# Kernel optimization log

Hardware: AMD Instinct MI355X
Metric: run time of the kernel (lower is better)

The kernel has to match this reference:

```python
import jax, jax.numpy as jnp
import numpy as np

B_, N, C, H = 512, 49, 256, 8
DH = C // H            # 32
RB, NRF = 8, 32
NWIN = B_ // RB        # 64
DC = 64                # class_token_dim
TC = C + 2 * DC        # 384
WS = 7
SCALE = DH ** -0.5


def _rel_pos_index():
    ch = np.arange(WS)
    coords = np.stack(np.meshgrid(ch, ch, indexing='ij')).reshape(2, -1)  # [2,49]
    rel = (coords[:, :, None] - coords[:, None, :]).transpose(1, 2, 0)    # [49,49,2]
    rel[..., 0] += WS - 1
    rel[..., 1] += WS - 1
    rel[..., 0] *= 2 * WS - 1
    return jnp.asarray(rel.sum(-1).reshape(-1))  # [49*49]


def _ln(x, axes, eps=1e-5):
    m = x.mean(axes, keepdims=True)
    v = x.var(axes, keepdims=True)
    return (x - m) * jax.lax.rsqrt(v + eps)


def setup_inputs() -> dict:
    key = jax.random.key(0)
    ks = jax.random.split(key, 20)
    def w(i, shape, s=0.02):
        return jax.random.normal(ks[i], shape, jnp.float32) * s
    return dict(
        x=w(0, (B_, N, C), 1.0),
        x_ref=w(1, (RB, NRF, C), 1.0),
        depth_token=w(2, (B_, N, DC), 1.0),
        seg_token=w(3, (B_, N, DC), 1.0),
        qkv_w=w(4, (C, 3 * C)), qkv_b=jnp.zeros(3 * C, jnp.float32),
        proj_w=w(5, (C, C)), proj_b=jnp.zeros(C, jnp.float32),
        rel_bias=w(6, ((2 * WS - 1) ** 2, H)),
        diff_mu=w(7, (1, 1, C), 1.0), diff_logsigma=w(8, (1, 1, C)),
        ref_qk_w=w(9, (C, 2 * C)), ref_qk_b=jnp.zeros(2 * C, jnp.float32),
        conv_w=w(10, (H, H, 3, 3), 0.1), conv_b=jnp.zeros(H, jnp.float32),
        q_norm_w=jnp.ones(C, jnp.float32), q_norm_b=jnp.zeros(C, jnp.float32),
        q_proj_w=w(11, (C, C)), q_proj_b=jnp.zeros(C, jnp.float32),
        cls_dth_q_w=w(12, (DC, DC)), cls_dth_q_b=jnp.zeros(DC, jnp.float32),
        cls_seg_q_w=w(13, (DC, DC)), cls_seg_q_b=jnp.zeros(DC, jnp.float32),
        global_k_w=w(14, (TC, TC)), global_k_b=jnp.zeros(TC, jnp.float32),
        global_v_w=w(15, (TC, TC)), global_v_b=jnp.zeros(TC, jnp.float32),
        proj_dth_w=w(16, (DC, DC)), proj_dth_b=jnp.zeros(DC, jnp.float32),
    )


def reference(x, x_ref, depth_token, seg_token, qkv_w, qkv_b, proj_w, proj_b,
              rel_bias, diff_mu, diff_logsigma, ref_qk_w, ref_qk_b, conv_w, conv_b,
              q_norm_w, q_norm_b, q_proj_w, q_proj_b, cls_dth_q_w, cls_dth_q_b,
              cls_seg_q_w, cls_seg_q_b, global_k_w, global_k_b, global_v_w,
              global_v_b, proj_dth_w, proj_dth_b):
    # qkv: [B_,N,3C] -> q,k,v each [B_,H,N,DH]
    qkv = (x @ qkv_w + qkv_b).reshape(B_, N, 3, H, DH).transpose(2, 0, 3, 1, 4)
    q, k, v = qkv[0], qkv[1], qkv[2]

    # ---- group attention (ref branch) ----
    ref_qk = (x_ref @ ref_qk_w + ref_qk_b).reshape(RB, NRF, 2, C).transpose(2, 0, 1, 3)
    ref_q, ref_v = ref_qk[0], ref_qk[1]                       # [RB,NRF,C]
    ref_q = diff_mu + jnp.exp(diff_logsigma) * ref_q
    ref_q = ref_q.reshape(RB, NRF, H, DH).transpose(0, 2, 1, 3)  # [RB,H,NRF,DH]
    ref_v = ref_v.reshape(RB, NRF, H, DH).transpose(0, 2, 1, 3)

    qs = (q * SCALE).reshape(RB, NWIN, H, N, DH)
    # scores against shared (per-image) ref keys; avoids materializing repeated K
    ref_attn = jnp.einsum('rwhnd,rhfd->rhwnf', qs, ref_q)     # [RB,H,NWIN,N,NRF]
    ref_attn_r = ref_attn.reshape(RB, H, NWIN * N, NRF)
    # 3-step diffusion: conv2d over heads-as-channels + LN(no affine) + gelu, residual
    for _ in range(3):
        u = jax.lax.conv_general_dilated(
            ref_attn_r, conv_w, (1, 1), 'SAME',
            dimension_numbers=('NCHW', 'OIHW', 'NCHW')) + conv_b[None, :, None, None]
        u = jax.nn.gelu(_ln(u, (-2, -1)), approximate=False)
        ref_attn_r = ref_attn_r + u
    ref_attn = jax.nn.softmax(ref_attn_r.reshape(RB, H, NWIN, N, NRF), axis=-1)
    q_new = jnp.einsum('rhwnf,rhfd->rwnhd', ref_attn, ref_v).reshape(B_, N, C)
    q_sc = q.transpose(0, 2, 1, 3).reshape(B_, N, C)          # unscaled shortcut
    q_new = (_ln(q_new + q_sc, (-1,)) * q_norm_w + q_norm_b) @ q_proj_w + q_proj_b + q_sc
    q_new = q_new.reshape(B_, N, H, DH).transpose(0, 2, 1, 3) * SCALE

    # ---- window attention with relative position bias ----
    bias = rel_bias[_rel_pos_index()].reshape(N, N, H).transpose(2, 0, 1)  # [H,N,N]
    attn = jax.nn.softmax(jnp.einsum('bhnd,bhmd->bhnm', q_new, k) + bias[None], axis=-1)
    out = jnp.einsum('bhnm,bhmd->bnhd', attn, v).reshape(B_, N, C)
    out = out @ proj_w + proj_b

    # ---- class-token global attention ----
    dch = DC // H   # 8
    tdh = TC // H   # 48
    depth_q = (depth_token @ cls_dth_q_w + cls_dth_q_b).reshape(B_, N, H, dch).transpose(0, 2, 1, 3) * SCALE
    seg_q = (seg_token @ cls_seg_q_w + cls_seg_q_b).reshape(B_, N, H, dch).transpose(0, 2, 1, 3) * SCALE
    t_x = jnp.concatenate([out, depth_token, seg_token], axis=-1)  # [B_,N,TC]
    t_k = (t_x @ global_k_w + global_k_b).reshape(B_, N, H, tdh).transpose(0, 2, 1, 3)
    t_v = (t_x @ global_v_w + global_v_b).reshape(B_, N, H, tdh).transpose(0, 2, 1, 3)

    d_attn = jax.nn.softmax(jnp.einsum('bhnc,bhnt->bhct', depth_q, t_k), axis=-1)
    d_tok = jnp.einsum('bhct,bhnt->bhcn', d_attn, t_v).reshape(B_, DC, N).transpose(0, 2, 1)
    d_tok = d_tok @ proj_dth_w + proj_dth_b
    s_attn = jax.nn.softmax(jnp.einsum('bhnc,bhnt->bhct', seg_q, t_k), axis=-1)
    s_tok = jnp.einsum('bhct,bhnt->bhcn', s_attn, t_v).reshape(B_, DC, N).transpose(0, 2, 1)
    s_tok = s_tok @ proj_dth_w + proj_dth_b  # NOTE: original uses proj_dth for seg too
    return out, d_tok, s_tok
```

## Files before the change

### kernel.cpp

```cpp
#include <hip/hip_runtime.h>
#include <hip/hip_bf16.h>

typedef __hip_bfloat16 bf16;
typedef short s16x8 __attribute__((ext_vector_type(8)));
typedef float f32x4 __attribute__((ext_vector_type(4)));
union V16 { uint4 u4; s16x8 s8; unsigned u[4]; unsigned short s[8]; };

static __device__ __forceinline__ float b2f(bf16 v){ return __bfloat162float(v); }
static __device__ __forceinline__ bf16  f2b(float v){ return __float2bfloat16(v); }
static __device__ __forceinline__ unsigned short f2bs(float x){
    union { float f; unsigned u; } c; c.f = x;
    unsigned r = c.u + 0x7fff + ((c.u >> 16) & 1);
    return (unsigned short)(r >> 16);
}
static __device__ __forceinline__ float bu2f(unsigned short b){
    union { unsigned u; float f; } c; c.u = ((unsigned)b) << 16; return c.f;
}
static __device__ __forceinline__ s16x8 ld16g(const bf16* p){
    V16 u; u.u4 = *(const uint4*)p; return u.s8;
}
static __device__ __forceinline__ void glds16(const void* g, void* l){
    __builtin_amdgcn_global_load_lds(
        (const __attribute__((address_space(1))) unsigned*)g,
        (__attribute__((address_space(3))) unsigned*)l, 16, 0, 0);
}

#define SCALE_T 0.17677669529663687f

__global__ __launch_bounds__(256) void prep_weights(
    const float* __restrict__ qkvw, const float* __restrict__ qpw,
    const float* __restrict__ pw,   const float* __restrict__ gkw,
    const float* __restrict__ gvw,  bf16* __restrict__ Wt)
{
    int idx = blockIdx.x * 256 + threadIdx.x;
    float v;
    if (idx < 196608)      { int j = idx;          int n = j >> 8, k = j & 255; v = qkvw[k * 768 + n]; }
    else if (idx < 262144) { int j = idx - 196608; int n = j >> 8, k = j & 255; v = qpw[k * 256 + n]; }
    else if (idx < 327680) { int j = idx - 262144; int n = j >> 8, k = j & 255; v = pw[k * 256 + n]; }
    else if (idx < 475136) { int j = idx - 327680; int n = j / 384, k = j - n * 384; v = gkw[k * 384 + n]; }
    else                   { int j = idx - 475136; int n = j / 384, k = j - n * 384; v = gvw[k * 384 + n]; }
    ((unsigned short*)Wt)[idx] = f2bs(v);
}

__global__ __launch_bounds__(256) void convert_f32_bf16(
    const float* __restrict__ in, bf16* __restrict__ out)
{
    int i = blockIdx.x * 256 + threadIdx.x;
    float4 v = ((const float4*)in)[i];
    ushort4 o;
    o.x = f2bs(v.x); o.y = f2bs(v.y); o.z = f2bs(v.z); o.w = f2bs(v.w);
    ((ushort4*)out)[i] = o;
}

template<int TOK>
__global__ __launch_bounds__(256, 4) void gemm_bb(
    const bf16* __restrict__ A, int lda,
    const float* __restrict__ tokD, const float* __restrict__ tokS,
    const bf16* __restrict__ Wt, const float* __restrict__ bias,
    const float* __restrict__ bias2,
    const bf16* __restrict__ addp, int addStride,
    float* __restrict__ outF, bf16* __restrict__ outB, int outStrideB,
    int K, int N, float scale)
{
    __shared__ char lds[2][16384];

    const int tid = threadIdx.x;
    const int wv = tid >> 6, lane = tid & 63;
    const int quad = lane >> 4, l15 = lane & 15;
    const int wr = wv >> 1, wc = wv & 1;

    const int gx = (int)gridDim.x;
    const int nwg = gx * (int)gridDim.y;
    int bid = (int)blockIdx.y * gx + (int)blockIdx.x;
    if ((nwg & 7) == 0) bid = (bid & 7) * (nwg >> 3) + (bid >> 3);
    const int bx = bid % gx, by = bid / gx;
    const int rowBase = by * 128, colBase = bx * 128;

    const int srow = tid >> 2;
    const int kOffE = (((tid & 3) ^ ((srow >> 1) & 3)) << 3);

    const unsigned swz = (unsigned)((quad ^ ((l15 >> 1) & 3)) << 4);
    const unsigned aoff0 = (unsigned)(wr * 4096 + l15 * 64) + swz;
    const unsigned boff0 = (unsigned)(wc * 4096 + l15 * 64) + swz;

    f32x4 acc[4][4];
    #pragma unroll
    for (int m = 0; m < 4; ++m)
        #pragma unroll
        for (int n = 0; n < 4; ++n)
            #pragma unroll
            for (int r = 0; r < 4; ++r) acc[m][n][r] = 0.f;

    auto stage = [&](int sbuf, int kt) {
        char* base = &lds[sbuf][0];
        #pragma unroll
        for (int c = 0; c < 2; ++c)
            glds16(Wt + (size_t)(colBase + c * 64 + srow) * K + (kt + kOffE),
                   base + 8192 + c * 4096 + tid * 16);
        if (!TOK || kt < 256) {
            #pragma unroll
            for (int c = 0; c < 2; ++c)
                glds16(A + (size_t)(rowBase + c * 64 + srow) * lda + (kt + kOffE),
                       base + c * 4096 + tid * 16);
        } else {
            #pragma unroll
            for (int c = 0; c < 2; ++c) {
                int row = rowBase + c * 64 + srow;
                const float* sf = (kt < 320)
                    ? (tokD + (size_t)row * 64 + (kt - 256 + kOffE))
                    : (tokS + (size_t)row * 64 + (kt - 320 + kOffE));
                float4 u0 = ((const float4*)sf)[0];
                float4 u1 = ((const float4*)sf)[1];
                V16 o;
                o.s[0] = f2bs(u0.x); o.s[1] = f2bs(u0.y);
                o.s[2] = f2bs(u0.z); o.s[3] = f2bs(u0.w);
                o.s[4] = f2bs(u1.x); o.s[5] = f2bs(u1.y);
                o.s[6] = f2bs(u1.z); o.s[7] = f2bs(u1.w);
                *(uint4*)(base + c * 4096 + tid * 16) = o.u4;
            }
        }
    };

    stage(0, 0);
    __syncthreads();
    int buf = 0;
    for (int kt = 0; kt < K; kt += 32) {
        if (kt + 32 < K) stage(buf ^ 1, kt + 32);
        const char* Ab2 = &lds[buf][0];
        const char* Bb2 = Ab2 + 8192;
        s16x8 af[4], bfr[4];
        #pragma unroll
        for (int m = 0; m < 4; ++m) af[m]  = *(const s16x8*)(Ab2 + aoff0 + m * 1024);
        #pragma unroll
        for (int n = 0; n < 4; ++n) bfr[n] = *(const s16x8*)(Bb2 + boff0 + n * 1024);
        #pragma unroll
        for (int m = 0; m < 4; ++m)
            #pragma unroll
            for (int n = 0; n < 4; ++n)
                acc[m][n] = __builtin_amdgcn_mfma_f32_16x16x32_bf16(af[m], bfr[n], acc[m][n], 0, 0, 0);
        __syncthreads();
        buf ^= 1;
    }

    if (outB) {
        #pragma unroll
        for (int n = 0; n < 4; ++n) {
            int col = colBase + wc * 64 + n * 16 + l15;
            float bb = bias2 ? (col < 384 ? bias[col] : bias2[col - 384]) : bias[col];
            #pragma unroll
            for (int m = 0; m < 4; ++m) {
                #pragma unroll
                for (int r = 0; r < 4; ++r) {
                    int rl = wr * 64 + m * 16 + quad * 4 + r;
                    float v = acc[m][n][r] + bb;
                    if (addp) v += b2f(addp[(size_t)(rowBase + rl) * addStride + col]);
                    v *= scale;
                    if (outF) outF[(size_t)(rowBase + rl) * N + col] = v;
                    int cbyte = (wc * 64 + n * 16 + l15) * 2;
                    int blk = ((cbyte >> 5) ^ ((rl >> 2) & 7)) & 7;
                    *(unsigned short*)((char*)lds + rl * 256 + (blk << 5) + (cbyte & 31)) = f2bs(v);
                }
            }
        }
        __syncthreads();
        #pragma unroll
        for (int i = 0; i < 8; ++i) {
            int lin = i * 256 + tid;
            int rl = lin >> 4, cb = lin & 15;
            int cb2 = ((((cb >> 1) ^ ((rl >> 2) & 7)) & 7) << 1) | (cb & 1);
            uint4 val = *(const uint4*)((const char*)lds + rl * 256 + cb2 * 16);
            *(uint4*)(outB + (size_t)(rowBase + rl) * outStrideB + colBase + cb * 8) = val;
        }
    } else {
        #pragma unroll
        for (int n = 0; n < 4; ++n) {
            int col = colBase + wc * 64 + n * 16 + l15;
            float bb = bias2 ? (col < 384 ? bias[col] : bias2[col - 384]) : bias[col];
            #pragma unroll
            for (int m = 0; m < 4; ++m) {
                #pragma unroll
                for (int r = 0; r < 4; ++r) {
                    int rl = wr * 64 + m * 16 + quad * 4 + r;
                    float v = acc[m][n][r] + bb;
                    if (addp) v += b2f(addp[(size_t)(rowBase + rl) * addStride + col]);
                    v *= scale;
                    if (outF) outF[(size_t)(rowBase + rl) * N + col] = v;
                }
            }
        }
    }
}

__global__ __launch_bounds__(256) void mfma_gemm(
    const void* __restrict__ A, int a_mode,
    const float* __restrict__ Xd, const float* __restrict__ Xs,
    const float* __restrict__ W, const float* __restrict__ bias,
    const bf16* __restrict__ addp, int addStride,
    float* __restrict__ outF, bf16* __restrict__ outB,
    int M, int K, int N, float scale)
{
    __shared__ __hip_bfloat16 Al[64][48];
    __shared__ __hip_bfloat16 Bl[64][48];

    const int tid  = threadIdx.x;
    const int wv   = tid >> 6, lane = tid & 63;
    const int quad = lane >> 4, l15 = lane & 15;
    const int rowBase = blockIdx.y * 64, colBase = blockIdx.x * 64;

    const int am = tid >> 2, ak = (tid & 3) * 8;
    const int bn = tid & 63, bk = (tid >> 6) * 8;

    f32x4 acc[4];
    #pragma unroll
    for (int t = 0; t < 4; ++t)
        #pragma unroll
        for (int r = 0; r < 4; ++r) acc[t][r] = 0.f;

    for (int kt = 0; kt < K; kt += 32) {
        s16x8 sa;
        if (a_mode == 1) {
            const bf16* Ab = (const bf16*)A;
            V16 u; u.u4 = *(const uint4*)(Ab + (size_t)(rowBase + am) * K + kt + ak);
            sa = u.s8;
        } else {
            const float* src; size_t base;
            if (a_mode == 0) {
                src = (const float*)A; base = (size_t)(rowBase + am) * K + kt + ak;
            } else {
                int kcol = kt + ak;
                if (kcol < 256)      { src = (const float*)A; base = (size_t)(rowBase + am) * 256 + kcol; }
                else if (kcol < 320) { src = Xd; base = (size_t)(rowBase + am) * 64 + (kcol - 256); }
                else                 { src = Xs; base = (size_t)(rowBase + am) * 64 + (kcol - 320); }
            }
            const float4* p = (const float4*)(src + base);
            float4 u0 = p[0], u1 = p[1];
            sa[0] = (short)f2bs(u0.x); sa[1] = (short)f2bs(u0.y);
            sa[2] = (short)f2bs(u0.z); sa[3] = (short)f2bs(u0.w);
            sa[4] = (short)f2bs(u1.x); sa[5] = (short)f2bs(u1.y);
            sa[6] = (short)f2bs(u1.z); sa[7] = (short)f2bs(u1.w);
        }
        *(s16x8*)&Al[am][ak] = sa;

        s16x8 sb;
        #pragma unroll
        for (int j = 0; j < 8; ++j)
            sb[j] = (short)f2bs(W[(size_t)(kt + bk + j) * N + colBase + bn]);
        *(s16x8*)&Bl[bn][bk] = sb;

        __syncthreads();

        s16x8 a = *(const s16x8*)&Al[wv * 16 + l15][quad * 8];
        #pragma unroll
        for (int t = 0; t < 4; ++t) {
            s16x8 b = *(const s16x8*)&Bl[t * 16 + l15][quad * 8];
            acc[t] = __builtin_amdgcn_mfma_f32_16x16x32_bf16(a, b, acc[t], 0, 0, 0);
        }
        __syncthreads();
    }

    #pragma unroll
    for (int t = 0; t < 4; ++t) {
        int col = colBase + t * 16 + l15;
        float bb = bias[col];
        #pragma unroll
        for (int r = 0; r < 4; ++r) {
            int row = rowBase + wv * 16 + quad * 4 + r;
            float v = acc[t][r] + bb;
            if (addp) v += b2f(addp[(size_t)row * addStride + col]);
            v *= scale;
            if (outF) outF[(size_t)row * N + col] = v;
            if (outB) outB[(size_t)row * N + col] = f2b(v);
        }
    }
}

__global__ __launch_bounds__(256) void refprep_kernel(
    const float* __restrict__ ref_qk, const float* __restrict__ mu,
    const float* __restrict__ ls, float* __restrict__ ref_q_t,
    float* __restrict__ ref_v_t)
{
    int idx = blockIdx.x * 256 + threadIdx.x;
    int d = idx & 31, f = (idx >> 5) & 31, h = (idx >> 10) & 7, r = idx >> 13;
    int c = h * 32 + d;
    size_t src = (size_t)(r * 32 + f) * 512 + c;
    ref_q_t[idx] = mu[c] + __expf(ls[c]) * ref_qk[src];
    ref_v_t[idx] = ref_qk[src + 256];
}

__global__ __launch_bounds__(256) void refattn_kernel(
    const bf16* __restrict__ qkv, const float* __restrict__ ref_q_t,
    bf16* __restrict__ ref_attn)
{
    int blk = blockIdx.x;
    int w = blk & 63, h = (blk >> 6) & 7, r = blk >> 9;
    int b = r * 64 + w;
    __shared__ float qt[49 * 32];
    __shared__ float rq[32 * 33];
    int tid = threadIdx.x;
    for (int l = tid; l < 1568; l += 256) {
        int n = l >> 5, d = l & 31;
        qt[l] = b2f(qkv[(size_t)(b * 49 + n) * 768 + h * 32 + d]) * SCALE_T;
    }
    for (int l = tid; l < 1024; l += 256) {
        int f = l >> 5, d = l & 31;
        rq[f * 33 + d] = ref_q_t[(size_t)((r * 8 + h) * 32 + f) * 32 + d];
    }
    __syncthreads();
    for (int l = tid; l < 1568; l += 256) {
        int n = l >> 5, f = l & 31;
        float acc = 0.f;
        #pragma unroll
        for (int d2 = 0; d2 < 32; ++d2) acc += qt[n * 32 + d2] * rq[f * 33 + d2];
        ref_attn[(size_t)(((r * 8 + h) * 64 + w) * 49 + n) * 32 + f] = f2b(acc);
    }
}

__global__ __launch_bounds__(256) void conv_kernel(
    const bf16* __restrict__ in, const float* __restrict__ conv_w,
    const float* __restrict__ conv_b, bf16* __restrict__ u)
{
    __shared__ float w_s[576];
    __shared__ float b_s[8];
    int tid = threadIdx.x;
    for (int l = tid; l < 576; l += 256) w_s[l] = conv_w[l];
    if (tid < 8) b_s[tid] = conv_b[tid];
    __syncthreads();

    int idx = blockIdx.x * 256 + tid;
    int fb = idx & 3;
    int p  = (idx >> 2) % 3136;
    int r  = idx / 12544;
    int f0 = fb * 8;

    float acc[8][8];
    #pragma unroll
    for (int o = 0; o < 8; ++o) {
        float bo = b_s[o];
        #pragma unroll
        for (int f = 0; f < 8; ++f) acc[o][f] = bo;
    }

    for (int i = 0; i < 8; ++i) {
        float ext[3][10];
        #pragma unroll
        for (int dy = 0; dy < 3; ++dy) {
            int pp = p + dy - 1;
            bool pv = (unsigned)pp < 3136u;
            size_t base = ((size_t)((r * 8 + i) * 3136 + (pv ? pp : 0))) * 32 + f0;
            V16 uv;
            uv.u4 = pv ? *(const uint4*)(in + base) : make_uint4(0, 0, 0, 0);
            #pragma unroll
            for (int j = 0; j < 8; ++j) {
                unsigned sh = uv.u[j >> 1];
                unsigned bits = (j & 1) ? (sh & 0xffff0000u) : (sh << 16);
                union { unsigned uu; float fl; } cv; cv.uu = bits;
                ext[dy][j + 1] = cv.fl;
            }
            ext[dy][0] = (pv && f0 > 0)      ? b2f(in[base - 1]) : 0.f;
            ext[dy][9] = (pv && f0 + 8 < 32) ? b2f(in[base + 8]) : 0.f;
        }
        #pragma unroll
        for (int o = 0; o < 8; ++o) {
            #pragma unroll
            for (int ky = 0; ky < 3; ++ky) {
                const float* wp = &w_s[((o * 8 + i) * 3 + ky) * 3];
                float w0 = wp[0], w1 = wp[1], w2 = wp[2];
                #pragma unroll
                for (int f = 0; f < 8; ++f)
                    acc[o][f] += ext[ky][f] * w0 + ext[ky][f + 1] * w1 + ext[ky][f + 2] * w2;
            }
        }
    }

    #pragma unroll
    for (int o = 0; o < 8; ++o) {
        bf16 ov[8];
        #pragma unroll
        for (int f = 0; f < 8; ++f) ov[f] = f2b(acc[o][f]);
        *(uint4*)(u + ((size_t)((r * 8 + o) * 3136 + p)) * 32 + f0) = *(uint4*)ov;
    }
}

__global__ __launch_bounds__(256) void lnstats_kernel(
    const bf16* __restrict__ u, float* __restrict__ stats4)
{
    int g4 = blockIdx.x;
    const bf16* p = u + (size_t)g4 * 25088;
    int tid = threadIdx.x;
    float s = 0.f, s2 = 0.f;
    for (int it = tid; it < 3136; it += 256) {
        V16 uv; uv.u4 = *(const uint4*)(p + it * 8);
        #pragma unroll
        for (int j = 0; j < 8; ++j) {
            unsigned sh = uv.u[j >> 1];
            unsigned bits = (j & 1) ? (sh & 0xffff0000u) : (sh << 16);
            union { unsigned uu; float fl; } cv; cv.uu = bits;
            s += cv.fl; s2 += cv.fl * cv.fl;
        }
    }
    __shared__ float r1[256], r2[256];
    r1[tid] = s; r2[tid] = s2; __syncthreads();
    for (int st = 128; st > 0; st >>= 1) {
        if (tid < st) { r1[tid] += r1[tid + st]; r2[tid] += r2[tid + st]; }
        __syncthreads();
    }
    if (tid == 0) {
        stats4[g4 * 2]     = r1[0];
        stats4[g4 * 2 + 1] = r2[0];
    }
}

__global__ __launch_bounds__(256) void lngelu_kernel(
    const bf16* __restrict__ u, const float* __restrict__ stats4,
    bf16* __restrict__ ref_attn)
{
    int idx8 = blockIdx.x * 256 + threadIdx.x;
    int g = idx8 / 12544;
    size_t base = (size_t)idx8 * 8;
    float sum = 0.f, sq = 0.f;
    #pragma unroll
    for (int q = 0; q < 4; ++q) {
        sum += stats4[(g * 4 + q) * 2];
        sq  += stats4[(g * 4 + q) * 2 + 1];
    }
    float mean = sum * (1.f / 100352.f);
    float var  = sq * (1.f / 100352.f) - mean * mean;
    var = fmaxf(var, 0.f);
    float rstd = rsqrtf(var + 1e-5f);
    V16 uv; uv.u4 = *(const uint4*)(u + base);
    V16 rv; rv.u4 = *(const uint4*)(ref_attn + base);
    bf16 outv[8];
    #pragma unroll
    for (int j = 0; j < 8; ++j) {
        unsigned shu = uv.u[j >> 1];
        unsigned shr = rv.u[j >> 1];
        unsigned bu = (j & 1) ? (shu & 0xffff0000u) : (shu << 16);
        unsigned br = (j & 1) ? (shr & 0xffff0000u) : (shr << 16);
        union { unsigned uu; float fl; } cu, cr; cu.uu = bu; cr.uu = br;
        float v = (cu.fl - mean) * rstd;
        float ge = 0.5f * v * (1.f + erff(v * 0.7071067811865476f));
        outv[j] = f2b(cr.fl + ge);
    }
    *(uint4*)(ref_attn + base) = *(uint4*)outv;
}

__global__ __launch_bounds__(256) void qnew_pre_kernel(
    const bf16* __restrict__ qkv, const bf16* __restrict__ ref_attn,
    const float* __restrict__ ref_v_t,
    const float* __restrict__ qnw, const float* __restrict__ qnb,
    bf16* __restrict__ ln_t)
{
    int ww = threadIdx.x >> 6, lane = threadIdx.x & 63;
    int row = blockIdx.x * 4 + ww;
    int b = row / 49, n = row % 49;
    int r = b >> 6, w = b & 63;
    int h = lane >> 3, d0 = (lane & 7) * 4;

    const bf16* la = ref_attn + ((size_t)(((r * 8 + h) * 64 + w) * 49 + n)) * 32 + d0;
    ushort4 lu = *(const ushort4*)la;
    float lg[4] = { bu2f(lu.x), bu2f(lu.y), bu2f(lu.z), bu2f(lu.w) };

    float m = fmaxf(fmaxf(lg[0], lg[1]), fmaxf(lg[2], lg[3]));
    m = fmaxf(m, __shfl_xor(m, 1));
    m = fmaxf(m, __shfl_xor(m, 2));
    m = fmaxf(m, __shfl_xor(m, 4));
    float p[4], s = 0.f;
    #pragma unroll
    for (int j = 0; j < 4; ++j) { p[j] = __expf(lg[j] - m); s += p[j]; }
    s += __shfl_xor(s, 1);
    s += __shfl_xor(s, 2);
    s += __shfl_xor(s, 4);
    float inv = 1.f / s;
    #pragma unroll
    for (int j = 0; j < 4; ++j) p[j] *= inv;

    const float* rv = ref_v_t + ((size_t)(r * 8 + h) * 32) * 32 + d0;
    float y[4] = {0.f, 0.f, 0.f, 0.f};
    #pragma unroll
    for (int f = 0; f < 32; ++f) {
        int src = (lane & 56) | (f >> 2);
        float pf = __shfl(p[f & 3], src);
        float4 rvf = *(const float4*)(rv + f * 32);
        y[0] += pf * rvf.x; y[1] += pf * rvf.y;
        y[2] += pf * rvf.z; y[3] += pf * rvf.w;
    }

    ushort4 qu = *(const ushort4*)(qkv + (size_t)row * 768 + lane * 4);
    float z[4] = { y[0] + bu2f(qu.x), y[1] + bu2f(qu.y),
                   y[2] + bu2f(qu.z), y[3] + bu2f(qu.w) };

    float s1 = z[0] + z[1] + z[2] + z[3];
    #pragma unroll
    for (int off = 1; off < 64; off <<= 1) s1 += __shfl_xor(s1, off);
    float mean = s1 * (1.f / 256.f);
    float zc[4] = { z[0] - mean, z[1] - mean, z[2] - mean, z[3] - mean };
    float s2 = zc[0]*zc[0] + zc[1]*zc[1] + zc[2]*zc[2] + zc[3]*zc[3];
    #pragma unroll
    for (int off = 1; off < 64; off <<= 1) s2 += __shfl_xor(s2, off);
    float rstd = rsqrtf(s2 * (1.f / 256.f) + 1e-5f);

    float4 wv = *(const float4*)(qnw + lane * 4);
    float4 bv = *(const float4*)(qnb + lane * 4);
    bf16 outv[4];
    outv[0] = f2b(zc[0] * rstd * wv.x + bv.x);
    outv[1] = f2b(zc[1] * rstd * wv.y + bv.y);
    outv[2] = f2b(zc[2] * rstd * wv.z + bv.z);
    outv[3] = f2b(zc[3] * rstd * wv.w + bv.w);
    *(ushort4*)(ln_t + (size_t)row * 256 + lane * 4) = *(ushort4*)outv;
}

__global__ __launch_bounds__(256) void winattn_kernel(
    const bf16* __restrict__ qkv, const bf16* __restrict__ q_new,
    const float* __restrict__ rel_bias, bf16* __restrict__ attn_out)
{
    const int wv = threadIdx.x >> 6, lane = threadIdx.x & 63;
    const int quad = lane >> 4, l15 = lane & 15;
    const int b = blockIdx.x >> 1;
    const int h = (blockIdx.x & 1) * 4 + wv;

    __shared__ bf16 lds[4 * 6912];
    bf16* P  = &lds[wv * 6912];
    bf16* vT = P + 4608;

    {
        int m = lane;
        if (m < 49) {
            const bf16* vp = qkv + ((size_t)(b * 49 + m)) * 768 + 512 + h * 32;
            V16 v0, v1, v2, v3;
            v0.u4 = *(const uint4*)(vp);
            v1.u4 = *(const uint4*)(vp + 8);
            v2.u4 = *(const uint4*)(vp + 16);
            v3.u4 = *(const uint4*)(vp + 24);
            #pragma unroll
            for (int d = 0; d < 8; ++d) {
                ((unsigned short*)vT)[d * 72 + m]        = v0.s[d];
                ((unsigned short*)vT)[(d + 8) * 72 + m]  = v1.s[d];
                ((unsigned short*)vT)[(d + 16) * 72 + m] = v2.s[d];
                ((unsigned short*)vT)[(d + 24) * 72 + m] = v3.s[d];
            }
        } else {
            #pragma unroll
            for (int d = 0; d < 32; ++d)
                ((unsigned short*)vT)[d * 72 + m] = 0;
        }
    }

    s16x8 aq[4], bk[4];
    #pragma unroll
    for (int t = 0; t < 4; ++t) {
        int qr = t * 16 + l15; qr = qr > 48 ? 48 : qr;
        aq[t] = ld16g(q_new + ((size_t)(b * 49 + qr)) * 256 + h * 32 + quad * 8);
        bk[t] = ld16g(qkv + ((size_t)(b * 49 + qr)) * 768 + 256 + h * 32 + quad * 8);
    }
    f32x4 S[4][4];
    #pragma unroll
    for (int tn = 0; tn < 4; ++tn)
        #pragma unroll
        for (int tm = 0; tm < 4; ++tm) {
            #pragma unroll
            for (int r = 0; r < 4; ++r) S[tn][tm][r] = 0.f;
            S[tn][tm] = __builtin_amdgcn_mfma_f32_16x16x32_bf16(aq[tn], bk[tm], S[tn][tm], 0, 0, 0);
        }

    int mvalid[4], mi[4], mj[4];
    #pragma unroll
    for (int tm = 0; tm < 4; ++tm) {
        int m0 = tm * 16 + l15;
        mvalid[tm] = (m0 < 49);
        int mc = m0 > 48 ? 48 : m0;
        mi[tm] = mc / 7; mj[tm] = mc - mi[tm] * 7;
    }
    #pragma unroll
    for (int tn = 0; tn < 4; ++tn) {
        #pragma unroll
        for (int r = 0; r < 4; ++r) {
            int n0 = tn * 16 + quad * 4 + r;
            int nc = n0 > 48 ? 48 : n0;
            int ni = nc / 7, nj = nc - (nc / 7) * 7;
            float vals[4];
            float mx = -1e30f;
            #pragma unroll
            for (int tm = 0; tm < 4; ++tm) {
                float v = S[tn][tm][r]
                        + rel_bias[((ni - mi[tm] + 6) * 13 + (nj - mj[tm] + 6)) * 8 + h];
                if (!mvalid[tm]) v = -1e30f;
                vals[tm] = v;
                mx = fmaxf(mx, v);
            }
            mx = fmaxf(mx, __shfl_xor(mx, 1));
            mx = fmaxf(mx, __shfl_xor(mx, 2));
            mx = fmaxf(mx, __shfl_xor(mx, 4));
            mx = fmaxf(mx, __shfl_xor(mx, 8));
            float s = 0.f;
            #pragma unroll
            for (int tm = 0; tm < 4; ++tm) { vals[tm] = __expf(vals[tm] - mx); s += vals[tm]; }
            s += __shfl_xor(s, 1);
            s += __shfl_xor(s, 2);
            s += __shfl_xor(s, 4);
            s += __shfl_xor(s, 8);
            float inv = 1.f / s;
            #pragma unroll
            for (int tm = 0; tm < 4; ++tm)
                ((unsigned short*)P)[n0 * 72 + tm * 16 + l15] = f2bs(vals[tm] * inv);
        }
    }

    f32x4 O[4][2];
    #pragma unroll
    for (int tn = 0; tn < 4; ++tn)
        #pragma unroll
        for (int td = 0; td < 2; ++td)
            #pragma unroll
            for (int r = 0; r < 4; ++r) O[tn][td][r] = 0.f;

    #pragma unroll
    for (int ks = 0; ks < 2; ++ks) {
        s16x8 bv0 = *(const s16x8*)&vT[(0 * 16 + l15) * 72 + ks * 32 + quad * 8];
        s16x8 bv1 = *(const s16x8*)&vT[(1 * 16 + l15) * 72 + ks * 32 + quad * 8];
        #pragma unroll
        for (int tn = 0; tn < 4; ++tn) {
            s16x8 ap = *(const s16x8*)&P[(tn * 16 + l15) * 72 + ks * 32 + quad * 8];
            O[tn][0] = __builtin_amdgcn_mfma_f32_16x16x32_bf16(ap, bv0, O[tn][0], 0, 0, 0);
            O[tn][1] = __builtin_amdgcn_mfma_f32_16x16x32_bf16(ap, bv1, O[tn][1], 0, 0, 0);
        }
    }

    #pragma unroll
    for (int tn = 0; tn < 4; ++tn)
        #pragma unroll
        for (int r = 0; r < 4; ++r) {
            int n0 = tn * 16 + quad * 4 + r;
            if (n0 < 49) {
                size_t base = ((size_t)(b * 49 + n0)) * 256 + h * 32;
                attn_out[base + l15]      = f2b(O[tn][0][r]);
                attn_out[base + 16 + l15] = f2b(O[tn][1][r]);
            }
        }
}

__global__ __launch_bounds__(256) void clsattn_kernel(
    const bf16* __restrict__ tkv,
    const bf16* __restrict__ depth_q, const bf16* __restrict__ seg_q,
    bf16* __restrict__ d_pre, bf16* __restrict__ s_pre)
{
    const int wv = threadIdx.x >> 6, lane = threadIdx.x & 63;
    const int quad = lane >> 4, l15 = lane & 15;
    const int bh = blockIdx.x * 4 + wv;
    const int b = bh >> 3, h = bh & 7;

    __shared__ bf16 lds[4 * 5760];
    unsigned short* QP = (unsigned short*)&lds[wv * 5760];
    unsigned short* KV = QP + 1152;

    {
        int n = lane;
        V16 dv, sv;
        if (n < 49) {
            dv.u4 = *(const uint4*)(depth_q + ((size_t)(b * 49 + n)) * 64 + h * 8);
            sv.u4 = *(const uint4*)(seg_q   + ((size_t)(b * 49 + n)) * 64 + h * 8);
        } else {
            dv.u4 = make_uint4(0, 0, 0, 0); sv.u4 = make_uint4(0, 0, 0, 0);
        }
        #pragma unroll
        for (int c = 0; c < 8; ++c) {
            QP[c * 72 + n]       = dv.s[c];
            QP[(8 + c) * 72 + n] = sv.s[c];
        }
    }
    {
        int n = lane;
        V16 k[6];
        if (n < 49) {
            const bf16* kp = tkv + ((size_t)(b * 49 + n)) * 768 + h * 48;
            #pragma unroll
            for (int c6 = 0; c6 < 6; ++c6) k[c6].u4 = *(const uint4*)(kp + c6 * 8);
        } else {
            #pragma unroll
            for (int c6 = 0; c6 < 6; ++c6) k[c6].u4 = make_uint4(0, 0, 0, 0);
        }
        #pragma unroll
        for (int c6 = 0; c6 < 6; ++c6)
            #pragma unroll
            for (int j = 0; j < 8; ++j)
                KV[(c6 * 8 + j) * 72 + n] = k[c6].s[j];
    }

    f32x4 S[3];
    #pragma unroll
    for (int t3 = 0; t3 < 3; ++t3)
        #pragma unroll
        for (int r = 0; r < 4; ++r) S[t3][r] = 0.f;
    #pragma unroll
    for (int ks = 0; ks < 2; ++ks) {
        s16x8 a = *(const s16x8*)&QP[l15 * 72 + ks * 32 + quad * 8];
        #pragma unroll
        for (int t3 = 0; t3 < 3; ++t3) {
            s16x8 bf = *(const s16x8*)&KV[(t3 * 16 + l15) * 72 + ks * 32 + quad * 8];
            S[t3] = __builtin_amdgcn_mfma_f32_16x16x32_bf16(a, bf, S[t3], 0, 0, 0);
        }
    }

    #pragma unroll
    for (int r = 0; r < 4; ++r) {
        float v0 = S[0][r], v1 = S[1][r], v2 = S[2][r];
        float mx = fmaxf(fmaxf(v0, v1), v2);
        mx = fmaxf(mx, __shfl_xor(mx, 1));
        mx = fmaxf(mx, __shfl_xor(mx, 2));
        mx = fmaxf(mx, __shfl_xor(mx, 4));
        mx = fmaxf(mx, __shfl_xor(mx, 8));
        float e0 = __expf(v0 - mx), e1 = __expf(v1 - mx), e2 = __expf(v2 - mx);
        float s = e0 + e1 + e2;
        s += __shfl_xor(s, 1);
        s += __shfl_xor(s, 2);
        s += __shfl_xor(s, 4);
        s += __shfl_xor(s, 8);
        float inv = 1.f / s;
        int c = quad * 4 + r;
        QP[c * 72 + 0 * 16 + l15] = f2bs(e0 * inv);
        QP[c * 72 + 1 * 16 + l15] = f2bs(e1 * inv);
        QP[c * 72 + 2 * 16 + l15] = f2bs(e2 * inv);
    }
    #pragma unroll
    for (int z = 0; z < 4; ++z)
        QP[(lane & 15) * 72 + 48 + (lane >> 4) * 4 + z] = 0;

    {
        int n = lane;
        V16 v[6], zv; zv.u4 = make_uint4(0, 0, 0, 0);
        if (n < 49) {
            const bf16* vp = tkv + ((size_t)(b * 49 + n)) * 768 + 384 + h * 48;
            #pragma unroll
            for (int c6 = 0; c6 < 6; ++c6) v[c6].u4 = *(const uint4*)(vp + c6 * 8);
        } else {
            #pragma unroll
            for (int c6 = 0; c6 < 6; ++c6) v[c6].u4 = zv.u4;
        }
        #pragma unroll
        for (int c6 = 0; c6 < 6; ++c6)
            *(uint4*)&KV[n * 72 + c6 * 8] = v[c6].u4;
        *(uint4*)&KV[n * 72 + 48] = zv.u4;
        *(uint4*)&KV[n * 72 + 56] = zv.u4;
    }

    f32x4 O[4];
    #pragma unroll
    for (int t4 = 0; t4 < 4; ++t4)
        #pragma unroll
        for (int r = 0; r < 4; ++r) O[t4][r] = 0.f;
    #pragma unroll
    for (int ks = 0; ks < 2; ++ks) {
        s16x8 a = *(const s16x8*)&QP[l15 * 72 + ks * 32 + quad * 8];
        #pragma unroll
        for (int t4 = 0; t4 < 4; ++t4) {
            s16x8 bf = *(const s16x8*)&KV[(t4 * 16 + l15) * 72 + ks * 32 + quad * 8];
            O[t4] = __builtin_amdgcn_mfma_f32_16x16x32_bf16(a, bf, O[t4], 0, 0, 0);
        }
    }

    #pragma unroll
    for (int t4 = 0; t4 < 4; ++t4) {
        int n = t4 * 16 + l15;
        if (n < 49) {
            size_t base = ((size_t)(b * 49 + n)) * 64 + h * 8;
            #pragma unroll
            for (int r = 0; r < 4; ++r) {
                int c = quad * 4 + r;
                if (c < 8) d_pre[base + c] = f2b(O[t4][r]);
                else       s_pre[base + c - 8] = f2b(O[t4][r]);
            }
        }
    }
}

extern "C" void kernel_launch(void* const* d_in, const int* in_sizes, int n_in,
                              void* d_out, int out_size, void* d_ws, size_t ws_size,
                              hipStream_t stream)
{
    const float* x          = (const float*)d_in[0];
    const float* x_ref      = (const float*)d_in[1];
    const float* dth_tok    = (const float*)d_in[2];
    const float* seg_tok    = (const float*)d_in[3];
    const float* qkv_w      = (const float*)d_in[4];
    const float* qkv_b      = (const float*)d_in[5];
    const float* proj_w     = (const float*)d_in[6];
    const float* proj_b     = (const float*)d_in[7];
    const float* rel_bias   = (const float*)d_in[8];
    const float* diff_mu    = (const float*)d_in[9];
    const float* diff_ls    = (const float*)d_in[10];
    const float* ref_qk_w   = (const float*)d_in[11];
    const float* ref_qk_b   = (const float*)d_in[12];
    const float* conv_w     = (const float*)d_in[13];
    const float* conv_b     = (const float*)d_in[14];
    const float* q_norm_w   = (const float*)d_in[15];
    const float* q_norm_b   = (const float*)d_in[16];
    const float* q_proj_w   = (const float*)d_in[17];
    const float* q_proj_b   = (const float*)d_in[18];
    const float* cls_dth_w  = (const float*)d_in[19];
    const float* cls_dth_b  = (const float*)d_in[20];
    const float* cls_seg_w  = (const float*)d_in[21];
    const float* cls_seg_b  = (const float*)d_in[22];
    const float* glob_k_w   = (const float*)d_in[23];
    const float* glob_k_b   = (const float*)d_in[24];
    const float* glob_v_w   = (const float*)d_in[25];
    const float* glob_v_b   = (const float*)d_in[26];
    const float* proj_dth_w = (const float*)d_in[27];
    const float* proj_dth_b = (const float*)d_in[28];

    bf16* wsb = (bf16*)d_ws;
    bf16* qkv      = wsb;
    bf16* tkv      = wsb;
    bf16* ref_attn = wsb + 19267584;
    bf16* q_new    = ref_attn;
    bf16* out0b    = ref_attn;
    bf16* depth_q  = ref_attn;
    bf16* seg_q    = ref_attn + 1605632;
    bf16* d_pre    = ref_attn + 3211264;
    bf16* s_pre    = ref_attn + 4816896;
    bf16* u_buf    = wsb + 25690112;
    bf16* xb       = u_buf;
    bf16* ln_t     = u_buf;
    bf16* attn_out = u_buf;
    float* ref_qk  = (float*)((char*)d_ws + 64225280);
    float* ref_q_t = ref_qk + 131072;
    float* ref_v_t = ref_q_t + 65536;
    float* stats4  = ref_qk;

    float* out0  = (float*)d_out;
    float* out_d = out0 + 6422528;
    float* out_s = out0 + 8028160;

    bf16* Wt_all = (bf16*)out_d;

    prep_weights<<<2432, 256, 0, stream>>>(qkv_w, q_proj_w, proj_w, glob_k_w, glob_v_w, Wt_all);
    convert_f32_bf16<<<6272, 256, 0, stream>>>(x, xb);

    gemm_bb<0><<<dim3(6, 196), 256, 0, stream>>>(xb, 256, nullptr, nullptr,
        Wt_all, qkv_b, nullptr, nullptr, 0, nullptr, qkv, 768, 256, 768, 1.f);
    mfma_gemm<<<dim3(8, 4), 256, 0, stream>>>(x_ref, 0, nullptr, nullptr, ref_qk_w, ref_qk_b,
                                              nullptr, 0, ref_qk, nullptr, 256, 256, 512, 1.f);
    refprep_kernel<<<256, 256, 0, stream>>>(ref_qk, diff_mu, diff_ls, ref_q_t, ref_v_t);
    refattn_kernel<<<4096, 256, 0, stream>>>(qkv, ref_q_t, ref_attn);
    for (int it = 0; it < 3; ++it) {
        conv_kernel<<<392, 256, 0, stream>>>(ref_attn, conv_w, conv_b, u_buf);
        lnstats_kernel<<<256, 256, 0, stream>>>(u_buf, stats4);
        lngelu_kernel<<<3136, 256, 0, stream>>>(u_buf, stats4, ref_attn);
    }
    qnew_pre_kernel<<<6272, 256, 0, stream>>>(qkv, ref_attn, ref_v_t,
                                              q_norm_w, q_norm_b, ln_t);
    gemm_bb<0><<<dim3(2, 196), 256, 0, stream>>>(ln_t, 256, nullptr, nullptr,
        Wt_all + 196608, q_proj_b, nullptr, qkv, 768, nullptr, q_new, 256, 256, 256, SCALE_T);
    winattn_kernel<<<1024, 256, 0, stream>>>(qkv, q_new, rel_bias, attn_out);
    gemm_bb<0><<<dim3(2, 196), 256, 0, stream>>>(attn_out, 256, nullptr, nullptr,
        Wt_all + 262144, proj_b, nullptr, nullptr, 0, out0, out0b, 256, 256, 256, 1.f);
    gemm_bb<1><<<dim3(6, 196), 256, 0, stream>>>(out0b, 256, dth_tok, seg_tok,
        Wt_all + 327680, glob_k_b, glob_v_b, nullptr, 0, nullptr, tkv, 768, 384, 768, 1.f);
    mfma_gemm<<<dim3(1, 392), 256, 0, stream>>>(dth_tok, 0, nullptr, nullptr, cls_dth_w, cls_dth_b,
                                                nullptr, 0, nullptr, depth_q, 25088, 64, 64, SCALE_T);
    mfma_gemm<<<dim3(1, 392), 256, 0, stream>>>(seg_tok, 0, nullptr, nullptr, cls_seg_w, cls_seg_b,
                                                nullptr, 0, nullptr, seg_q, 25088, 64, 64, SCALE_T);
    clsattn_kernel<<<1024, 256, 0, stream>>>(tkv, depth_q, seg_q, d_pre, s_pre);
    mfma_gemm<<<dim3(1, 392), 256, 0, stream>>>(d_pre, 1, nullptr, nullptr, proj_dth_w, proj_dth_b,
                                                nullptr, 0, out_d, nullptr, 25088, 64, 64, 1.f);
    mfma_gemm<<<dim3(1, 392), 256, 0, stream>>>(s_pre, 1, nullptr, nullptr, proj_dth_w, proj_dth_b,
                                                nullptr, 0, out_s, nullptr, 25088, 64, 64, 1.f);
}
```

Baseline: 494.0 us.

## Fuse LN stats into conv, batch small 64x64 GEMMs, pre-convert class tokens

The conv kernel now computes the per-group sum and sum-of-squares and atomically accumulates them, which removes the separate lnstats pass over u_buf in each of the three iterations. refattn zeroes the stats buffers. The four 64x64 mfma_gemm launches are replaced by two launches of a small64 kernel that handles two tasks per grid, keeps the transposed weight in LDS and does the dot products with MFMA. The depth and seg tokens are converted to bf16 once in a new kernel, so the global k/v GEMM can load them with async global-to-LDS copies. The costs are atomic contention and a bf16 token buffer aliased into out_s.

```diff
diff --git a/kernel.cpp b/kernel.cpp
--- a/kernel.cpp
+++ b/kernel.cpp
@@ -52,10 +52,27 @@
     ((ushort4*)out)[i] = o;
 }
 
+__global__ __launch_bounds__(256) void tok2b_kernel(
+    const float* __restrict__ dth, const float* __restrict__ seg,
+    bf16* __restrict__ tokb)
+{
+    int i = blockIdx.x * 256 + threadIdx.x;
+    int row = i >> 4, j8 = i & 15;
+    const float* src = (j8 < 8) ? (dth + (size_t)row * 64 + j8 * 8)
+                                : (seg + (size_t)row * 64 + (j8 - 8) * 8);
+    float4 u0 = ((const float4*)src)[0];
+    float4 u1 = ((const float4*)src)[1];
+    V16 o;
+    o.s[0] = f2bs(u0.x); o.s[1] = f2bs(u0.y);
+    o.s[2] = f2bs(u0.z); o.s[3] = f2bs(u0.w);
+    o.s[4] = f2bs(u1.x); o.s[5] = f2bs(u1.y);
+    o.s[6] = f2bs(u1.z); o.s[7] = f2bs(u1.w);
+    *(uint4*)(tokb + (size_t)row * 128 + j8 * 8) = o.u4;
+}
+
 template<int TOK>
 __global__ __launch_bounds__(256, 4) void gemm_bb(
-    const bf16* __restrict__ A, int lda,
-    const float* __restrict__ tokD, const float* __restrict__ tokS,
+    const bf16* __restrict__ A, int lda, const bf16* __restrict__ A2,
     const bf16* __restrict__ Wt, const float* __restrict__ bias,
     const float* __restrict__ bias2,
     const bf16* __restrict__ addp, int addStride,
@@ -104,20 +121,9 @@
                        base + c * 4096 + tid * 16);
         } else {
             #pragma unroll
-            for (int c = 0; c < 2; ++c) {
-                int row = rowBase + c * 64 + srow;
-                const float* sf = (kt < 320)
-                    ? (tokD + (size_t)row * 64 + (kt - 256 + kOffE))
-                    : (tokS + (size_t)row * 64 + (kt - 320 + kOffE));
-                float4 u0 = ((const float4*)sf)[0];
-                float4 u1 = ((const float4*)sf)[1];
-                V16 o;
-                o.s[0] = f2bs(u0.x); o.s[1] = f2bs(u0.y);
-                o.s[2] = f2bs(u0.z); o.s[3] = f2bs(u0.w);
-                o.s[4] = f2bs(u1.x); o.s[5] = f2bs(u1.y);
-                o.s[6] = f2bs(u1.z); o.s[7] = f2bs(u1.w);
-                *(uint4*)(base + c * 4096 + tid * 16) = o.u4;
-            }
+            for (int c = 0; c < 2; ++c)
+                glds16(A2 + (size_t)(rowBase + c * 64 + srow) * 128 + (kt - 256 + kOffE),
+                       base + c * 4096 + tid * 16);
         }
     };
 
@@ -191,11 +197,86 @@
     }
 }
 
+template<int AF32, int OF32>
+__global__ __launch_bounds__(256) void small64(
+    const void* __restrict__ a0, const void* __restrict__ a1,
+    const float* __restrict__ w0, const float* __restrict__ w1,
+    const float* __restrict__ b0, const float* __restrict__ b1,
+    void* __restrict__ o0, void* __restrict__ o1, float scale)
+{
+    __shared__ unsigned short WT[64 * 72];
+    __shared__ float bsh[64];
+    const int task = blockIdx.y;
+    const void*  A    = task ? a1 : a0;
+    const float* W    = task ? w1 : w0;
+    const float* bias = task ? b1 : b0;
+    void*        outp = task ? o1 : o0;
+
+    int tid = threadIdx.x;
+    for (int l = tid; l < 4096; l += 256) {
+        int k = l >> 6, n = l & 63;
+        WT[n * 72 + k] = f2bs(W[l]);
+    }
+    if (tid < 64) bsh[tid] = bias[tid];
+    __syncthreads();
+
+    const int wv = tid >> 6, lane = tid & 63;
+    const int quad = lane >> 4, l15 = lane & 15;
+    const int rowBase = blockIdx.x * 64;
+    const int arow = rowBase + wv * 16 + l15;
+
+    s16x8 a[2];
+    if (AF32) {
+        const float* Ar = (const float*)A + (size_t)arow * 64;
+        #pragma unroll
+        for (int ks = 0; ks < 2; ++ks) {
+            float4 u0 = *(const float4*)(Ar + ks * 32 + quad * 8);
+            float4 u1 = *(const float4*)(Ar + ks * 32 + quad * 8 + 4);
+            V16 o;
+            o.s[0] = f2bs(u0.x); o.s[1] = f2bs(u0.y);
+            o.s[2] = f2bs(u0.z); o.s[3] = f2bs(u0.w);
+            o.s[4] = f2bs(u1.x); o.s[5] = f2bs(u1.y);
+            o.s[6] = f2bs(u1.z); o.s[7] = f2bs(u1.w);
+            a[ks] = o.s8;
+        }
+    } else {
+        const bf16* Ar = (const bf16*)A + (size_t)arow * 64;
+        #pragma unroll
+        for (int ks = 0; ks < 2; ++ks)
+            a[ks] = ld16g(Ar + ks * 32 + quad * 8);
+    }
+
+    f32x4 acc[4];
+    #pragma unroll
+    for (int n = 0; n < 4; ++n)
+        #pragma unroll
+        for (int r = 0; r < 4; ++r) acc[n][r] = 0.f;
+
+    #pragma unroll
+    for (int ks = 0; ks < 2; ++ks)
+        #pragma unroll
+        for (int n = 0; n < 4; ++n) {
+            s16x8 b = *(const s16x8*)&WT[(n * 16 + l15) * 72 + ks * 32 + quad * 8];
+            acc[n] = __builtin_amdgcn_mfma_f32_16x16x32_bf16(a[ks], b, acc[n], 0, 0, 0);
+        }
+
+    #pragma unroll
+    for (int n = 0; n < 4; ++n) {
+        int col = n * 16 + l15;
+        float bb = bsh[col];
+        #pragma unroll
+        for (int r = 0; r < 4; ++r) {
+            int row = rowBase + wv * 16 + quad * 4 + r;
+            float v = (acc[n][r] + bb) * scale;
+            if (OF32) ((float*)outp)[(size_t)row * 64 + col] = v;
+            else      ((bf16*)outp)[(size_t)row * 64 + col] = f2b(v);
+        }
+    }
+}
+
 __global__ __launch_bounds__(256) void mfma_gemm(
     const void* __restrict__ A, int a_mode,
-    const float* __restrict__ Xd, const float* __restrict__ Xs,
     const float* __restrict__ W, const float* __restrict__ bias,
-    const bf16* __restrict__ addp, int addStride,
     float* __restrict__ outF, bf16* __restrict__ outB,
     int M, int K, int N, float scale)
 {
@@ -223,16 +304,8 @@
             V16 u; u.u4 = *(const uint4*)(Ab + (size_t)(rowBase + am) * K + kt + ak);
             sa = u.s8;
         } else {
-            const float* src; size_t base;
-            if (a_mode == 0) {
-                src = (const float*)A; base = (size_t)(rowBase + am) * K + kt + ak;
-            } else {
-                int kcol = kt + ak;
-                if (kcol < 256)      { src = (const float*)A; base = (size_t)(rowBase + am) * 256 + kcol; }
-                else if (kcol < 320) { src = Xd; base = (size_t)(rowBase + am) * 64 + (kcol - 256); }
-                else                 { src = Xs; base = (size_t)(rowBase + am) * 64 + (kcol - 320); }
-            }
-            const float4* p = (const float4*)(src + base);
+            const float* src = (const float*)A;
+            const float4* p = (const float4*)(src + (size_t)(rowBase + am) * K + kt + ak);
             float4 u0 = p[0], u1 = p[1];
             sa[0] = (short)f2bs(u0.x); sa[1] = (short)f2bs(u0.y);
             sa[2] = (short)f2bs(u0.z); sa[3] = (short)f2bs(u0.w);
@@ -265,9 +338,7 @@
         #pragma unroll
         for (int r = 0; r < 4; ++r) {
             int row = rowBase + wv * 16 + quad * 4 + r;
-            float v = acc[t][r] + bb;
-            if (addp) v += b2f(addp[(size_t)row * addStride + col]);
-            v *= scale;
+            float v = (acc[t][r] + bb) * scale;
             if (outF) outF[(size_t)row * N + col] = v;
             if (outB) outB[(size_t)row * N + col] = f2b(v);
         }
@@ -289,14 +360,15 @@
 
 __global__ __launch_bounds__(256) void refattn_kernel(
     const bf16* __restrict__ qkv, const float* __restrict__ ref_q_t,
-    bf16* __restrict__ ref_attn)
+    bf16* __restrict__ ref_attn, float* __restrict__ statsA)
 {
     int blk = blockIdx.x;
+    int tid = threadIdx.x;
+    if (blk == 0 && tid < 384) statsA[tid] = 0.f;
     int w = blk & 63, h = (blk >> 6) & 7, r = blk >> 9;
     int b = r * 64 + w;
     __shared__ float qt[49 * 32];
     __shared__ float rq[32 * 33];
-    int tid = threadIdx.x;
     for (int l = tid; l < 1568; l += 256) {
         int n = l >> 5, d = l & 31;
         qt[l] = b2f(qkv[(size_t)(b * 49 + n) * 768 + h * 32 + d]) * SCALE_T;
@@ -317,10 +389,12 @@
 
 __global__ __launch_bounds__(256) void conv_kernel(
     const bf16* __restrict__ in, const float* __restrict__ conv_w,
-    const float* __restrict__ conv_b, bf16* __restrict__ u)
+    const float* __restrict__ conv_b, bf16* __restrict__ u,
+    float* __restrict__ statsIt)
 {
     __shared__ float w_s[576];
     __shared__ float b_s[8];
+    __shared__ float red1[4][8], red2[4][8];
     int tid = threadIdx.x;
     for (int l = tid; l < 576; l += 256) w_s[l] = conv_w[l];
     if (tid < 8) b_s[tid] = conv_b[tid];
@@ -372,57 +446,51 @@
         }
     }
 
+    float so[8], s2o[8];
     #pragma unroll
     for (int o = 0; o < 8; ++o) {
         bf16 ov[8];
-        #pragma unroll
-        for (int f = 0; f < 8; ++f) ov[f] = f2b(acc[o][f]);
+        float s = 0.f, s2 = 0.f;
+        #pragma unroll
+        for (int f = 0; f < 8; ++f) {
+            ov[f] = f2b(acc[o][f]);
+            s += acc[o][f]; s2 += acc[o][f] * acc[o][f];
+        }
+        so[o] = s; s2o[o] = s2;
         *(uint4*)(u + ((size_t)((r * 8 + o) * 3136 + p)) * 32 + f0) = *(uint4*)ov;
     }
-}
-
-__global__ __launch_bounds__(256) void lnstats_kernel(
-    const bf16* __restrict__ u, float* __restrict__ stats4)
-{
-    int g4 = blockIdx.x;
-    const bf16* p = u + (size_t)g4 * 25088;
-    int tid = threadIdx.x;
-    float s = 0.f, s2 = 0.f;
-    for (int it = tid; it < 3136; it += 256) {
-        V16 uv; uv.u4 = *(const uint4*)(p + it * 8);
-        #pragma unroll
-        for (int j = 0; j < 8; ++j) {
-            unsigned sh = uv.u[j >> 1];
-            unsigned bits = (j & 1) ? (sh & 0xffff0000u) : (sh << 16);
-            union { unsigned uu; float fl; } cv; cv.uu = bits;
-            s += cv.fl; s2 += cv.fl * cv.fl;
-        }
-    }
-    __shared__ float r1[256], r2[256];
-    r1[tid] = s; r2[tid] = s2; __syncthreads();
-    for (int st = 128; st > 0; st >>= 1) {
-        if (tid < st) { r1[tid] += r1[tid + st]; r2[tid] += r2[tid + st]; }
-        __syncthreads();
-    }
-    if (tid == 0) {
-        stats4[g4 * 2]     = r1[0];
-        stats4[g4 * 2 + 1] = r2[0];
+
+    #pragma unroll
+    for (int o = 0; o < 8; ++o) {
+        #pragma unroll
+        for (int off = 32; off > 0; off >>= 1) {
+            so[o]  += __shfl_xor(so[o],  off);
+            s2o[o] += __shfl_xor(s2o[o], off);
+        }
+    }
+    int wv = tid >> 6, lane = tid & 63;
+    if (lane == 0) {
+        #pragma unroll
+        for (int o = 0; o < 8; ++o) { red1[wv][o] = so[o]; red2[wv][o] = s2o[o]; }
+    }
+    __syncthreads();
+    if (tid < 8) {
+        float s = red1[0][tid] + red1[1][tid] + red1[2][tid] + red1[3][tid];
+        float s2 = red2[0][tid] + red2[1][tid] + red2[2][tid] + red2[3][tid];
+        int g = r * 8 + tid;
+        atomicAdd(&statsIt[g * 2], s);
+        atomicAdd(&statsIt[g * 2 + 1], s2);
     }
 }
 
 __global__ __launch_bounds__(256) void lngelu_kernel(
-    const bf16* __restrict__ u, const float* __restrict__ stats4,
+    const bf16* __restrict__ u, const float* __restrict__ statsIt,
     bf16* __restrict__ ref_attn)
 {
     int idx8 = blockIdx.x * 256 + threadIdx.x;
     int g = idx8 / 12544;
     size_t base = (size_t)idx8 * 8;
-    float sum = 0.f, sq = 0.f;
-    #pragma unroll
-    for (int q = 0; q < 4; ++q) {
-        sum += stats4[(g * 4 + q) * 2];
-        sq  += stats4[(g * 4 + q) * 2 + 1];
-    }
+    float sum = statsIt[g * 2], sq = statsIt[g * 2 + 1];
     float mean = sum * (1.f / 100352.f);
     float var  = sq * (1.f / 100352.f) - mean * mean;
     var = fmaxf(var, 0.f);
@@ -823,44 +891,41 @@
     float* ref_qk  = (float*)((char*)d_ws + 64225280);
     float* ref_q_t = ref_qk + 131072;
     float* ref_v_t = ref_q_t + 65536;
-    float* stats4  = ref_qk;
+    float* statsA  = ref_qk;
 
     float* out0  = (float*)d_out;
     float* out_d = out0 + 6422528;
     float* out_s = out0 + 8028160;
 
     bf16* Wt_all = (bf16*)out_d;
+    bf16* tokb   = (bf16*)out_s;
 
     prep_weights<<<2432, 256, 0, stream>>>(qkv_w, q_proj_w, proj_w, glob_k_w, glob_v_w, Wt_all);
     convert_f32_bf16<<<6272, 256, 0, stream>>>(x, xb);
-
-    gemm_bb<0><<<dim3(6, 196), 256, 0, stream>>>(xb, 256, nullptr, nullptr,
+    tok2b_kernel<<<1568, 256, 0, stream>>>(dth_tok, seg_tok, tokb);
+
+    gemm_bb<0><<<dim3(6, 196), 256, 0, stream>>>(xb, 256, nullptr,
         Wt_all, qkv_b, nullptr, nullptr, 0, nullptr, qkv, 768, 256, 768, 1.f);
-    mfma_gemm<<<dim3(8, 4), 256, 0, stream>>>(x_ref, 0, nullptr, nullptr, ref_qk_w, ref_qk_b,
-                                              nullptr, 0, ref_qk, nullptr, 256, 256, 512, 1.f);
+    mfma_gemm<<<dim3(8, 4), 256, 0, stream>>>(x_ref, 0, ref_qk_w, ref_qk_b,
+                                              ref_qk, nullptr, 256, 256, 512, 1.f);
     refprep_kernel<<<256, 256, 0, stream>>>(ref_qk, diff_mu, diff_ls, ref_q_t, ref_v_t);
-    refattn_kernel<<<4096, 256, 0, stream>>>(qkv, ref_q_t, ref_attn);
+    refattn_kernel<<<4096, 256, 0, stream>>>(qkv, ref_q_t, ref_attn, statsA);
     for (int it = 0; it < 3; ++it) {
-        conv_kernel<<<392, 256, 0, stream>>>(ref_attn, conv_w, conv_b, u_buf);
-        lnstats_kernel<<<256, 256, 0, stream>>>(u_buf, stats4);
-        lngelu_kernel<<<3136, 256, 0, stream>>>(u_buf, stats4, ref_attn);
+        conv_kernel<<<392, 256, 0, stream>>>(ref_attn, conv_w, conv_b, u_buf, statsA + it * 128);
+        lngelu_kernel<<<3136, 256, 0, stream>>>(u_buf, statsA + it * 128, ref_attn);
     }
     qnew_pre_kernel<<<6272, 256, 0, stream>>>(qkv, ref_attn, ref_v_t,
                                               q_norm_w, q_norm_b, ln_t);
-    gemm_bb<0><<<dim3(2, 196), 256, 0, stream>>>(ln_t, 256, nullptr, nullptr,
+    gemm_bb<0><<<dim3(2, 196), 256, 0, stream>>>(ln_t, 256, nullptr,
         Wt_all + 196608, q_proj_b, nullptr, qkv, 768, nullptr, q_new, 256, 256, 256, SCALE_T);
     winattn_kernel<<<1024, 256, 0, stream>>>(qkv, q_new, rel_bias, attn_out);
-    gemm_bb<0><<<dim3(2, 196), 256, 0, stream>>>(attn_out, 256, nullptr, nullptr,
+    gemm_bb<0><<<dim3(2, 196), 256, 0, stream>>>(attn_out, 256, nullptr,
         Wt_all + 262144, proj_b, nullptr, nullptr, 0, out0, out0b, 256, 256, 256, 1.f);
-    gemm_bb<1><<<dim3(6, 196), 256, 0, stream>>>(out0b, 256, dth_tok, seg_tok,
+    gemm_bb<1><<<dim3(6, 196), 256, 0, stream>>>(out0b, 256, tokb,
         Wt_all + 327680, glob_k_b, glob_v_b, nullptr, 0, nullptr, tkv, 768, 384, 768, 1.f);
-    mfma_gemm<<<dim3(1, 392), 256, 0, stream>>>(dth_tok, 0, nullptr, nullptr, cls_dth_w, cls_dth_b,
-                                                nullptr, 0, nullptr, depth_q, 25088, 64, 64, SCALE_T);
-    mfma_gemm<<<dim3(1, 392), 256, 0, stream>>>(seg_tok, 0, nullptr, nullptr, cls_seg_w, cls_seg_b,
-                                                nullptr, 0, nullptr, seg_q, 25088, 64, 64, SCALE_T);
+    small64<1, 0><<<dim3(392, 2), 256, 0, stream>>>(dth_tok, seg_tok,
+        cls_dth_w, cls_seg_w, cls_dth_b, cls_seg_b, depth_q, seg_q, SCALE_T);
     clsattn_kernel<<<1024, 256, 0, stream>>>(tkv, depth_q, seg_q, d_pre, s_pre);
-    mfma_gemm<<<dim3(1, 392), 256, 0, stream>>>(d_pre, 1, nullptr, nullptr, proj_dth_w, proj_dth_b,
-                                                nullptr, 0, out_d, nullptr, 25088, 64, 64, 1.f);
-    mfma_gemm<<<dim3(1, 392), 256, 0, stream>>>(s_pre, 1, nullptr, nullptr, proj_dth_w, proj_dth_b,
-                                                nullptr, 0, out_s, nullptr, 25088, 64, 64, 1.f);
-}
+    small64<0, 1><<<dim3(392, 2), 256, 0, stream>>>(d_pre, s_pre,
+        proj_dth_w, proj_dth_w, proj_dth_b, proj_dth_b, out_d, out_s, 1.f);
+}
```

Result: slower. 517.2 us (+4.7%).
